# Kernel optimization log

Hardware: AMD Instinct MI355X
Metric: run time of the kernel (lower is better)

The kernel has to match this reference:

```python
import jax, jax.numpy as jnp
import numpy as np

D_MODEL = 512
N_HEADS = 8
D_K = D_MODEL // N_HEADS


def setup_inputs() -> dict:
    key = jax.random.key(0)
    ks = jax.random.split(key, 11)
    B, L, D = 2, 4096, D_MODEL
    s = 1.0 / np.sqrt(D)
    return {
        "q": jax.random.normal(ks[0], (B, L, D), jnp.float32),
        "k": jax.random.normal(ks[1], (B, L, D), jnp.float32),
        "v": jax.random.normal(ks[2], (B, L, D), jnp.float32),
        "Wq": jax.random.normal(ks[3], (D, D), jnp.float32) * s,
        "bq": jnp.zeros((D,), jnp.float32),
        "Wk": jax.random.normal(ks[4], (D, D), jnp.float32) * s,
        "bk": jnp.zeros((D,), jnp.float32),
        "Wv": jax.random.normal(ks[5], (D, D), jnp.float32) * s,
        "bv": jnp.zeros((D,), jnp.float32),
        "Wo": jax.random.normal(ks[6], (D, D), jnp.float32) * s,
        "bo": jnp.zeros((D,), jnp.float32),
    }


def reference(q, k, v, Wq, bq, Wk, bk, Wv, bv, Wo, bo):
    B, L, D = q.shape
    H, dk = N_HEADS, D_K
    # projections -> [B, H, L, dk]
    qh = (q @ Wq + bq).reshape(B, L, H, dk).transpose(0, 2, 1, 3)
    kh = (k @ Wk + bk).reshape(B, -1, H, dk).transpose(0, 2, 1, 3)
    vh = (v @ Wv + bv).reshape(B, -1, H, dk).transpose(0, 2, 1, 3)
    scores = jnp.einsum("bhqd,bhkd->bhqk", qh, kh) / jnp.sqrt(jnp.float32(dk))
    attn = jax.nn.softmax(scores, axis=-1)  # dropout: eval-mode identity
    ctx = jnp.einsum("bhqk,bhkd->bhqd", attn, vh)
    ctx = ctx.transpose(0, 2, 1, 3).reshape(B, L, D)
    return ctx @ Wo + bo
```

## Files before the change

kernel.cpp:

```cpp
#include <hip/hip_runtime.h>
#include <hip/hip_bf16.h>

#define NB 2
#define NL 4096
#define ND 512
#define NH 8
#define NDK 64
#define NM (NB * NL)
#define QSCALE 0.18033688011112042f

typedef short bf16x8_t __attribute__((ext_vector_type(8)));
typedef float f32x4_t __attribute__((ext_vector_type(4)));

static __device__ __forceinline__ unsigned short f2bs(float f) {
  union { float f; unsigned u; } c; c.f = f;
  unsigned r = c.u + 0x7fffu + ((c.u >> 16) & 1u);
  return (unsigned short)(r >> 16);
}
static __device__ __forceinline__ float bs2f(unsigned short s) {
  union { unsigned u; float f; } c; c.u = ((unsigned)s) << 16; return c.f;
}
static __device__ __forceinline__ unsigned pk_bf16(float a, float b) {
  union { __hip_bfloat162 h; unsigned u; } c;
  c.h = __float22bfloat162_rn(make_float2(a, b));
  return c.u;
}
static __device__ __forceinline__ unsigned cvt_pk_hw(float a, float b) {
  unsigned r;
  asm("v_cvt_pk_bf16_f32 %0, %1, %2" : "=v"(r) : "v"(a), "v"(b));
  return r;
}
static __device__ __forceinline__ void split_pk(float a, float b,
                                                unsigned& hw, unsigned& lw) {
  const unsigned short ha = f2bs(a), hb = f2bs(b);
  hw = (unsigned)ha | ((unsigned)hb << 16);
  lw = (unsigned)f2bs(a - bs2f(ha)) | ((unsigned)f2bs(b - bs2f(hb)) << 16);
}

struct WArgs {
  const float* W[4];
  unsigned short* Th[4];
  unsigned short* Tl[4];
};
__global__ __launch_bounds__(256)
void wsplit_kernel(WArgs a)
{
  const int z = blockIdx.z;
  const float* __restrict__ W = a.W[z];
  const int tid = threadIdx.x;
  const int n = blockIdx.x * 64 + (tid & 63);
  const int kb = blockIdx.y * 64 + (tid >> 6) * 16;
  unsigned short h[16], l[16];
#pragma unroll
  for (int u = 0; u < 16; ++u) {
    const float x = W[(size_t)(kb + u) * ND + n];
    h[u] = f2bs(x);
    l[u] = f2bs(x - bs2f(h[u]));
  }
  unsigned wh[8], wl[8];
#pragma unroll
  for (int p = 0; p < 8; ++p) {
    wh[p] = (unsigned)h[2 * p] | ((unsigned)h[2 * p + 1] << 16);
    wl[p] = (unsigned)l[2 * p] | ((unsigned)l[2 * p + 1] << 16);
  }
  unsigned short* th = a.Th[z] + (size_t)n * ND + kb;
  unsigned short* tl = a.Tl[z] + (size_t)n * ND + kb;
  *(uint4*)th = make_uint4(wh[0], wh[1], wh[2], wh[3]);
  *(uint4*)(th + 8) = make_uint4(wh[4], wh[5], wh[6], wh[7]);
  *(uint4*)tl = make_uint4(wl[0], wl[1], wl[2], wl[3]);
  *(uint4*)(tl + 8) = make_uint4(wl[4], wl[5], wl[6], wl[7]);
}

template <bool ASPLIT, int NJ, int OUTMODE, int WI, int WJ, bool AFP32, bool AMERGE>
__device__ __forceinline__ void gemm_core(
    const void* __restrict__ Ahi_, const unsigned short* __restrict__ Alo,
    const unsigned short* __restrict__ Bh, const unsigned short* __restrict__ Bl,
    const float* __restrict__ bias, unsigned short* __restrict__ outH,
    float* __restrict__ outF, int m0, int n0, float scale,
    const float* __restrict__ opA, const float* __restrict__ lpA)
{
  static_assert(!(ASPLIT && AFP32), "unsupported combo");
  static_assert(!(AFP32 && AMERGE), "unsupported combo");
  constexpr int WGC = NJ / WJ;
  static_assert((4 / WGC) * WI * 16 == 128, "wave grid must tile 128 rows");
  static_assert(OUTMODE == 1 || (WI == 4 && WJ == 4 && WGC == 2),
                "epilogues 0/2 assume 2x2 wave grid");

  __shared__ unsigned short AH[128][36];
  __shared__ unsigned short AL[ASPLIT ? 128 : 1][36];
  __shared__ unsigned short BHs[NJ * 16][36];
  __shared__ unsigned short BLs[NJ * 16][36];

  const int tid = threadIdx.x;
  const int lane = tid & 63, w = tid >> 6;
  const int m = lane & 15, quad = lane >> 4;
  const int wr = w / WGC, wc = w % WGC;
  const int r = tid >> 1, hf = (tid & 1) * 16;
  const int rb = (NJ == 8) ? (tid >> 1) : (tid >> 2);
  const int cb = (NJ == 8) ? ((tid & 1) * 16) : ((tid & 3) * 8);

  const unsigned short* aRow = nullptr;
  const float* aRowF = nullptr;
  if constexpr (AFP32)
    aRowF = (const float*)Ahi_ + (size_t)(m0 + r) * ND + hf;
  else if constexpr (!AMERGE)
    aRow = (const unsigned short*)Ahi_ + (size_t)(m0 + r) * ND + hf;
  const unsigned short* alRow =
      (ASPLIT && !AMERGE) ? (Alo + (size_t)(m0 + r) * ND + hf) : nullptr;
  const unsigned short* bhRow = Bh + (size_t)(n0 + rb) * ND + cb;
  const unsigned short* blRow = Bl + (size_t)(n0 + rb) * ND + cb;

  int abb = 0, all = 0;
  if constexpr (AMERGE) {
    abb = (m0 + r) >> 12;
    all = (m0 + r) & (NL - 1);
  }

  uint4 ra0, ra1;
  float4 fa0, fa1, fa2, fa3;
  if constexpr (AFP32) {
    fa0 = *(const float4*)(aRowF);
    fa1 = *(const float4*)(aRowF + 4);
    fa2 = *(const float4*)(aRowF + 8);
    fa3 = *(const float4*)(aRowF + 12);
  } else if constexpr (!AMERGE) {
    ra0 = *(const uint4*)(aRow);
    ra1 = *(const uint4*)(aRow + 8);
  }
  uint4 rl0, rl1;
  if constexpr (ASPLIT && !AMERGE) {
    rl0 = *(const uint4*)(alRow);
    rl1 = *(const uint4*)(alRow + 8);
  }
  uint4 rbh0 = *(const uint4*)(bhRow);
  uint4 rbl0 = *(const uint4*)(blRow);
  uint4 rbh1, rbl1;
  if constexpr (NJ == 8) {
    rbh1 = *(const uint4*)(bhRow + 8);
    rbl1 = *(const uint4*)(blRow + 8);
  }

  f32x4_t acc[WI][WJ];
#pragma unroll
  for (int i = 0; i < WI; ++i)
#pragma unroll
    for (int j = 0; j < WJ; ++j) acc[i][j] = (f32x4_t){0.f, 0.f, 0.f, 0.f};

  for (int k0 = 0; k0 < ND; k0 += 32) {
    float4 a00, a01, a02, a03, a10, a11, a12, a13;
    float li0, li1;
    if constexpr (AMERGE) {
      const int kk = k0 + hf;
      const int head = kk >> 6;
      const int d0 = kk & (NDK - 1);
      const size_t prow = (size_t)(abb * 8 + head) * NL + all;
      const float* p0 = opA + prow * NDK + d0;
      const float* p1 = p0 + (size_t)16 * NL * NDK;
      a00 = *(const float4*)p0;
      a01 = *(const float4*)(p0 + 4);
      a02 = *(const float4*)(p0 + 8);
      a03 = *(const float4*)(p0 + 12);
      a10 = *(const float4*)p1;
      a11 = *(const float4*)(p1 + 4);
      a12 = *(const float4*)(p1 + 8);
      a13 = *(const float4*)(p1 + 12);
      li0 = lpA[prow];
      li1 = lpA[prow + (size_t)16 * NL];
    }
    __syncthreads();
    if constexpr (AMERGE) {
      const float inv = 1.0f / (li0 + li1);
      uint4 uh0, ul0, uh1, ul1;
      split_pk((a00.x + a10.x) * inv, (a00.y + a10.y) * inv, uh0.x, ul0.x);
      split_pk((a00.z + a10.z) * inv, (a00.w + a10.w) * inv, uh0.y, ul0.y);
      split_pk((a01.x + a11.x) * inv, (a01.y + a11.y) * inv, uh0.z, ul0.z);
      split_pk((a01.z + a11.z) * inv, (a01.w + a11.w) * inv, uh0.w, ul0.w);
      split_pk((a02.x + a12.x) * inv, (a02.y + a12.y) * inv, uh1.x, ul1.x);
      split_pk((a02.z + a12.z) * inv, (a02.w + a12.w) * inv, uh1.y, ul1.y);
      split_pk((a03.x + a13.x) * inv, (a03.y + a13.y) * inv, uh1.z, ul1.z);
      split_pk((a03.z + a13.z) * inv, (a03.w + a13.w) * inv, uh1.w, ul1.w);
      *(uint4*)&AH[r][hf] = uh0;
      *(uint4*)&AH[r][hf + 8] = uh1;
      *(uint4*)&AL[r][hf] = ul0;
      *(uint4*)&AL[r][hf + 8] = ul1;
    } else if constexpr (AFP32) {
      uint4 ua0, ua1;
      ua0.x = pk_bf16(fa0.x, fa0.y);
      ua0.y = pk_bf16(fa0.z, fa0.w);
      ua0.z = pk_bf16(fa1.x, fa1.y);
      ua0.w = pk_bf16(fa1.z, fa1.w);
      ua1.x = pk_bf16(fa2.x, fa2.y);
      ua1.y = pk_bf16(fa2.z, fa2.w);
      ua1.z = pk_bf16(fa3.x, fa3.y);
      ua1.w = pk_bf16(fa3.z, fa3.w);
      *(uint4*)&AH[r][hf] = ua0;
      *(uint4*)&AH[r][hf + 8] = ua1;
    } else {
      *(uint4*)&AH[r][hf] = ra0;
      *(uint4*)&AH[r][hf + 8] = ra1;
    }
    if constexpr (ASPLIT && !AMERGE) {
      *(uint4*)&AL[r][hf] = rl0;
      *(uint4*)&AL[r][hf + 8] = rl1;
    }
    *(uint4*)&BHs[rb][cb] = rbh0;
    *(uint4*)&BLs[rb][cb] = rbl0;
    if constexpr (NJ == 8) {
      *(uint4*)&BHs[rb][cb + 8] = rbh1;
      *(uint4*)&BLs[rb][cb + 8] = rbl1;
    }
    if (k0 + 32 < ND) {
      const int kn = k0 + 32;
      if constexpr (AFP32) {
        fa0 = *(const float4*)(aRowF + kn);
        fa1 = *(const float4*)(aRowF + kn + 4);
        fa2 = *(const float4*)(aRowF + kn + 8);
        fa3 = *(const float4*)(aRowF + kn + 12);
      } else if constexpr (!AMERGE) {
        ra0 = *(const uint4*)(aRow + kn);
        ra1 = *(const uint4*)(aRow + kn + 8);
      }
      if constexpr (ASPLIT && !AMERGE) {
        rl0 = *(const uint4*)(alRow + kn);
        rl1 = *(const uint4*)(alRow + kn + 8);
      }
      rbh0 = *(const uint4*)(bhRow + kn);
      rbl0 = *(const uint4*)(blRow + kn);
      if constexpr (NJ == 8) {
        rbh1 = *(const uint4*)(bhRow + kn + 8);
        rbl1 = *(const uint4*)(blRow + kn + 8);
      }
    }
    __syncthreads();

    bf16x8_t ah[WI], al[ASPLIT ? WI : 1];
#pragma unroll
    for (int i = 0; i < WI; ++i) {
      ah[i] = *(const bf16x8_t*)&AH[wr * (WI * 16) + 16 * i + m][quad * 8];
      if constexpr (ASPLIT)
        al[i] = *(const bf16x8_t*)&AL[wr * (WI * 16) + 16 * i + m][quad * 8];
    }
#pragma unroll
    for (int j = 0; j < WJ; ++j) {
      const bf16x8_t bhj = *(const bf16x8_t*)&BHs[16 * (wc * WJ + j) + m][quad * 8];
      const bf16x8_t blj = *(const bf16x8_t*)&BLs[16 * (wc * WJ + j) + m][quad * 8];
#pragma unroll
      for (int i = 0; i < WI; ++i) {
        acc[i][j] = __builtin_amdgcn_mfma_f32_16x16x32_bf16(ah[i], bhj, acc[i][j], 0, 0, 0);
        acc[i][j] = __builtin_amdgcn_mfma_f32_16x16x32_bf16(ah[i], blj, acc[i][j], 0, 0, 0);
        if constexpr (ASPLIT)
          acc[i][j] = __builtin_amdgcn_mfma_f32_16x16x32_bf16(al[i], bhj, acc[i][j], 0, 0, 0);
      }
    }
  }

  if constexpr (OUTMODE == 1) {
#pragma unroll
    for (int i = 0; i < WI; ++i)
#pragma unroll
      for (int rr = 0; rr < 4; ++rr) {
        const int mg = m0 + wr * (WI * 16) + 16 * i + quad * 4 + rr;
#pragma unroll
        for (int j = 0; j < WJ; ++j) {
          const int n = n0 + 16 * (wc * WJ + j) + m;
          outF[(size_t)mg * ND + n] = (acc[i][j][rr] + bias[n]) * scale;
        }
      }
  } else if constexpr (OUTMODE == 0) {
    unsigned short* T = &BHs[0][0];
    const int bb = m0 >> 12;
#pragma unroll
    for (int p = 0; p < 4; ++p) {
      __syncthreads();
      if (wr == (p >> 1)) {
#pragma unroll
        for (int i2 = 0; i2 < 2; ++i2) {
          const int i = (p & 1) * 2 + i2;
#pragma unroll
          for (int j = 0; j < WJ; ++j) {
            const int n = wc * 64 + 16 * j + m;
            const float bv = bias[n0 + n];
#pragma unroll
            for (int rr = 0; rr < 4; ++rr)
              T[(16 * i2 + quad * 4 + rr) * 136 + n] =
                  f2bs((acc[i][j][rr] + bv) * scale);
          }
        }
      }
      __syncthreads();
      const int lr = tid >> 3;
      const int seg = tid & 7;
      const uint4 t0 = *(const uint4*)&T[lr * 136 + seg * 16];
      const uint4 t1 = *(const uint4*)&T[lr * 136 + seg * 16 + 8];
      const int ng = n0 + seg * 16;
      const int h = ng >> 6, d = ng & (NDK - 1);
      const int l = (m0 + p * 32 + lr) & (NL - 1);
      unsigned short* dp = outH + (((size_t)(bb * NH + h)) * NL + l) * NDK + d;
      *(uint4*)dp = t0;
      *(uint4*)(dp + 8) = t1;
    }
  } else {
    unsigned short* T = &BHs[0][0];
    const int bb = m0 >> 12;
    const int lbase = m0 & (NL - 1);
#pragma unroll
    for (int p = 0; p < 4; ++p) {
      __syncthreads();
      if (wr == (p >> 1)) {
#pragma unroll
        for (int i2 = 0; i2 < 2; ++i2) {
          const int i = (p & 1) * 2 + i2;
#pragma unroll
          for (int j = 0; j < WJ; ++j) {
            const int n = wc * 64 + 16 * j + m;
            const float bv = bias[n0 + n];
            const unsigned w0 = pk_bf16((acc[i][j][0] + bv) * scale,
                                        (acc[i][j][1] + bv) * scale);
            const unsigned w1 = pk_bf16((acc[i][j][2] + bv) * scale,
                                        (acc[i][j][3] + bv) * scale);
            *(uint2*)&T[n * 34 + 16 * i2 + quad * 4] = make_uint2(w0, w1);
          }
        }
      }
      __syncthreads();
      const int n = tid >> 1;
      const int l0 = (tid & 1) * 16;
      const uint4 t0 = *(const uint4*)&T[n * 34 + l0];
      const uint4 t1 = *(const uint4*)&T[n * 34 + l0 + 8];
      const int ng = n0 + n;
      const int h = ng >> 6, d = ng & (NDK - 1);
      unsigned short* dp =
          outH + (((size_t)(bb * NH + h)) * NDK + d) * NL + lbase + 32 * p + l0;
      *(uint4*)dp = t0;
      *(uint4*)(dp + 8) = t1;
    }
  }
}

struct ProjArgs {
  const float* A[3];
  const unsigned short* Bh[3];
  const unsigned short* Bl[3];
  const float* bias[3];
  unsigned short* out[3];
  float scale[3];
};
__global__ __launch_bounds__(256, 3)
void gemm_proj_kernel(ProjArgs a)
{
  const int z = blockIdx.z;
  if (z < 2)
    gemm_core<false, 8, 0, 4, 4, true, false>(
        a.A[z], nullptr, a.Bh[z], a.Bl[z], a.bias[z], a.out[z], nullptr,
        blockIdx.x * 128, blockIdx.y * 128, a.scale[z], nullptr, nullptr);
  else
    gemm_core<false, 8, 2, 4, 4, true, false>(
        a.A[2], nullptr, a.Bh[2], a.Bl[2], a.bias[2], a.out[2], nullptr,
        blockIdx.x * 128, blockIdx.y * 128, a.scale[2], nullptr, nullptr);
}
__global__ __launch_bounds__(256, 3)
void gemm_out_kernel(const float* __restrict__ opA, const float* __restrict__ lpA,
                     const unsigned short* __restrict__ Bh,
                     const unsigned short* __restrict__ Bl,
                     const float* __restrict__ bias, float* __restrict__ out)
{
  gemm_core<true, 4, 1, 2, 4, false, true>(
      nullptr, nullptr, Bh, Bl, bias, nullptr, out,
      blockIdx.x * 128, blockIdx.y * 64, 1.0f, opA, lpA);
}

__global__ __launch_bounds__(256, 2)
void attn_kernel(const unsigned short* __restrict__ qh, const unsigned short* __restrict__ kh,
                 const unsigned short* __restrict__ vt_g, float* __restrict__ op,
                 float* __restrict__ lp)
{
  __shared__ unsigned short Ks[2][64 * 64];
  __shared__ unsigned short Vt[2][64 * 64];

  const int tid = threadIdx.x;
  const int w = tid >> 6;
  const int lane = tid & 63;
  const int m = lane & 15;
  const int quad = lane >> 4;
  const int sw = m & 7;

  const int bid = blockIdx.x;
  const int half = bid & 1;
  const int qt = (bid >> 1) & 15;
  const int bh = bid >> 5;
  const int kt0 = half * 32, kt1 = kt0 + 32;
  const unsigned short* qb = qh + (size_t)bh * NL * NDK;
  const unsigned short* kb = kh + (size_t)bh * NL * NDK;
  const unsigned short* vb = vt_g + (size_t)bh * NDK * NL;

  bf16x8_t aq[4][2];
#pragma unroll
  for (int mt = 0; mt < 4; ++mt) {
    const unsigned short* qsrc =
        qb + (size_t)(qt * 256 + w * 64 + mt * 16 + m) * NDK + quad * 8;
    aq[mt][0] = *(const bf16x8_t*)(qsrc);
    aq[mt][1] = *(const bf16x8_t*)(qsrc + 32);
  }

  const short ob = (short)0x3F80;
  const bf16x8_t ones = {ob, ob, ob, ob, ob, ob, ob, ob};

  f32x4_t o[4][4];
#pragma unroll
  for (int mt = 0; mt < 4; ++mt)
#pragma unroll
    for (int nt = 0; nt < 4; ++nt) o[mt][nt] = (f32x4_t){0.f, 0.f, 0.f, 0.f};
  f32x4_t ol[4];
#pragma unroll
  for (int mt = 0; mt < 4; ++mt) ol[mt] = (f32x4_t){0.f, 0.f, 0.f, 0.f};

  const int kr = tid >> 2;
  const int kcb = tid & 3;
  const int kc = kcb * 16;
  const int r7 = kr & 7;
  const int st0 = kr * 64 + ((2 * kcb) ^ r7) * 8;
  const int st1 = kr * 64 + ((2 * kcb + 1) ^ r7) * 8;

  const int rowb = m * 64;
  const int ck0 = rowb + ((quad ^ sw) * 8);
  const int ck1 = rowb + (((quad + 4) ^ sw) * 8);
  const int vq = quad >> 1, vo = (quad & 1) * 4;
  const int va0[2] = { rowb + vo + (((0 + vq) ^ sw) * 8),
                       rowb + vo + (((4 + vq) ^ sw) * 8) };
  const int va1[2] = { rowb + vo + (((2 + vq) ^ sw) * 8),
                       rowb + vo + (((6 + vq) ^ sw) * 8) };

  const unsigned short* kptr = kb + (size_t)(kt0 * 64 + kr) * NDK + kc;
  const unsigned short* vptr = vb + (size_t)kr * NL + kt0 * 64 + kc;
  uint4 pk0 = *(const uint4*)kptr;
  uint4 pk1 = *(const uint4*)(kptr + 8);
  uint4 pv0 = *(const uint4*)vptr;
  uint4 pv1 = *(const uint4*)(vptr + 8);
  *(uint4*)&Ks[0][st0] = pk0;
  *(uint4*)&Ks[0][st1] = pk1;
  *(uint4*)&Vt[0][st0] = pv0;
  *(uint4*)&Vt[0][st1] = pv1;
  kptr += 64 * NDK;
  vptr += 64;
  pk0 = *(const uint4*)kptr;
  pk1 = *(const uint4*)(kptr + 8);
  pv0 = *(const uint4*)vptr;
  pv1 = *(const uint4*)(vptr + 8);
  __syncthreads();

#define ATTN_STEP(B, W, KT)                                                   \
  {                                                                           \
            \
    f32x4_t s[4][4];                                            \
    _Pragma("unroll")                                                         \
    for (int nt = 0; nt < 4; ++nt) {                                          \
      const bf16x8_t kf0 = *(const bf16x8_t*)&Ks[B][nt * 1024 + ck0];         \
      const bf16x8_t kf1 = *(const bf16x8_t*)&Ks[B][nt * 1024 + ck1];         \
      _Pragma("unroll")                                                       \
      for (int mt = 0; mt < 4; ++mt) {                                        \
        f32x4_t s_ = (f32x4_t){0.f, 0.f, 0.f, 0.f};                           \
        s_ = __builtin_amdgcn_mfma_f32_16x16x32_bf16(kf0, aq[mt][0], s_, 0, 0, 0); \
        s_ = __builtin_amdgcn_mfma_f32_16x16x32_bf16(kf1, aq[mt][1], s_, 0, 0, 0); \
        s[nt][mt] = s_;                                                       \
      }                                                                       \
    }                                                                         \
    __builtin_amdgcn_sched_barrier(0);   \
    _Pragma("unroll")                                                         \
    for (int c = 0; c < 2; ++c) {                                             \
      union U { bf16x8_t v; unsigned d[4]; };                                 \
      U pa[4];                                                                \
      _Pragma("unroll")                                                       \
      for (int mt = 0; mt < 4; ++mt) {                                        \
        pa[mt].d[0] = cvt_pk_hw(__builtin_amdgcn_exp2f(s[2 * c][mt][0]),      \
                                __builtin_amdgcn_exp2f(s[2 * c][mt][1]));     \
        pa[mt].d[1] = cvt_pk_hw(__builtin_amdgcn_exp2f(s[2 * c][mt][2]),      \
                                __builtin_amdgcn_exp2f(s[2 * c][mt][3]));     \
        pa[mt].d[2] = cvt_pk_hw(__builtin_amdgcn_exp2f(s[2 * c + 1][mt][0]),  \
                                __builtin_amdgcn_exp2f(s[2 * c + 1][mt][1])); \
        pa[mt].d[3] = cvt_pk_hw(__builtin_amdgcn_exp2f(s[2 * c + 1][mt][2]),  \
                                __builtin_amdgcn_exp2f(s[2 * c + 1][mt][3])); \
      }                                                                       \
      __builtin_amdgcn_s_setprio(1);                                          \
      _Pragma("unroll")                                                       \
      for (int nt = 0; nt < 4; ++nt) {                                        \
        union { bf16x8_t v; uint2 h[2]; } vf;                                 \
        vf.h[0] = *(const uint2*)&Vt[B][nt * 1024 + va0[c]];                  \
        vf.h[1] = *(const uint2*)&Vt[B][nt * 1024 + va1[c]];                  \
        _Pragma("unroll")                                                     \
        for (int mt = 0; mt < 4; ++mt)                                        \
          o[mt][nt] = __builtin_amdgcn_mfma_f32_16x16x32_bf16(pa[mt].v, vf.v, \
                                                              o[mt][nt], 0, 0, 0); \
      }                                                                       \
      _Pragma("unroll")                                                       \
      for (int mt = 0; mt < 4; ++mt)                                          \
        ol[mt] = __builtin_amdgcn_mfma_f32_16x16x32_bf16(pa[mt].v, ones,      \
                                                         ol[mt], 0, 0, 0);    \
      __builtin_amdgcn_s_setprio(0);                                          \
    }                                                                         \
    if ((KT) + 1 < kt1) {                                                     \
      *(uint4*)&Ks[W][st0] = pk0;                                             \
      *(uint4*)&Ks[W][st1] = pk1;                                             \
      *(uint4*)&Vt[W][st0] = pv0;                                             \
      *(uint4*)&Vt[W][st1] = pv1;                                             \
      if ((KT) + 2 < kt1) {                                                   \
        kptr += 64 * NDK;                                                     \
        vptr += 64;                                                           \
        pk0 = *(const uint4*)kptr;                                            \
        pk1 = *(const uint4*)(kptr + 8);                                      \
        pv0 = *(const uint4*)vptr;                                            \
        pv1 = *(const uint4*)(vptr + 8);                                      \
      }                                                                       \
      __syncthreads();                                                        \
    }                                                                         \
  }

  for (int kt = kt0; kt < kt1; kt += 2) {
    ATTN_STEP(0, 1, kt);
    ATTN_STEP(1, 0, kt + 1);
  }
#undef ATTN_STEP

  const size_t pbase = (size_t)(half * 16 + bh) * NL;
#pragma unroll
  for (int mt = 0; mt < 4; ++mt) {
    const int q0 = qt * 256 + w * 64 + mt * 16 + quad * 4;
    if (m == 0)
      *(float4*)&lp[pbase + q0] =
          make_float4(ol[mt][0], ol[mt][1], ol[mt][2], ol[mt][3]);
#pragma unroll
    for (int r = 0; r < 4; ++r) {
      float* dst = op + (pbase + q0 + r) * NDK;
#pragma unroll
      for (int nt = 0; nt < 4; ++nt) dst[16 * nt + m] = o[mt][nt][r];
    }
  }
}

extern "C" void kernel_launch(void* const* d_in, const int* in_sizes, int n_in,
                              void* d_out, int out_size, void* d_ws, size_t ws_size,
                              hipStream_t stream)
{
  const float* q  = (const float*)d_in[0];
  const float* k  = (const float*)d_in[1];
  const float* v  = (const float*)d_in[2];
  const float* Wq = (const float*)d_in[3];
  const float* bq = (const float*)d_in[4];
  const float* Wk = (const float*)d_in[5];
  const float* bk = (const float*)d_in[6];
  const float* Wv = (const float*)d_in[7];
  const float* bv = (const float*)d_in[8];
  const float* Wo = (const float*)d_in[9];
  const float* bo = (const float*)d_in[10];

  const size_t PLANE = (size_t)NM * ND;
  unsigned short* wt = (unsigned short*)d_ws;
  unsigned short* qhp = wt + 8 * (size_t)ND * ND;
  unsigned short* khp = qhp + PLANE;
  unsigned short* vtp = khp + PLANE;
  float* op = (float*)(vtp + PLANE);
  float* lp = op + 2 * (size_t)16 * NL * NDK;

  unsigned short* wth[4], *wtl[4];
  for (int i = 0; i < 4; ++i) {
    wth[i] = wt + (size_t)(2 * i) * ND * ND;
    wtl[i] = wt + (size_t)(2 * i + 1) * ND * ND;
  }

  WArgs wa;
  wa.W[0] = Wq; wa.W[1] = Wk; wa.W[2] = Wv; wa.W[3] = Wo;
  for (int i = 0; i < 4; ++i) { wa.Th[i] = wth[i]; wa.Tl[i] = wtl[i]; }
  wsplit_kernel<<<dim3(8, 8, 4), 256, 0, stream>>>(wa);

  ProjArgs pa;
  pa.A[0] = q; pa.A[1] = k; pa.A[2] = v;
  pa.Bh[0] = wth[0]; pa.Bl[0] = wtl[0];
  pa.Bh[1] = wth[1]; pa.Bl[1] = wtl[1];
  pa.Bh[2] = wth[2]; pa.Bl[2] = wtl[2];
  pa.bias[0] = bq; pa.bias[1] = bk; pa.bias[2] = bv;
  pa.out[0] = qhp; pa.out[1] = khp; pa.out[2] = vtp;
  pa.scale[0] = QSCALE; pa.scale[1] = 1.0f; pa.scale[2] = 1.0f;
  gemm_proj_kernel<<<dim3(NM / 128, ND / 128, 3), 256, 0, stream>>>(pa);

  attn_kernel<<<dim3(NB * NH * (NL / 256) * 2), 256, 0, stream>>>(qhp, khp, vtp, op, lp);

  gemm_out_kernel<<<dim3(NM / 128, ND / 64), 256, 0, stream>>>(
      op, lp, wth[3], wtl[3], bo, (float*)d_out);
}
```

Before: 243.5 us.

## Stream B tiles directly into double-buffered LDS via global_load_lds

```diff
diff --git a/kernel.cpp b/kernel.cpp
--- a/kernel.cpp
+++ b/kernel.cpp
@@ -35,6 +35,11 @@
   const unsigned short ha = f2bs(a), hb = f2bs(b);
   hw = (unsigned)ha | ((unsigned)hb << 16);
   lw = (unsigned)f2bs(a - bs2f(ha)) | ((unsigned)f2bs(b - bs2f(hb)) << 16);
+}
+static __device__ __forceinline__ void gload_lds16(const void* g, void* l) {
+  __builtin_amdgcn_global_load_lds(
+      (const __attribute__((address_space(1))) unsigned*)g,
+      (__attribute__((address_space(3))) unsigned*)l, 16, 0, 0);
 }
 
 struct WArgs {
@@ -85,19 +90,21 @@
   static_assert((4 / WGC) * WI * 16 == 128, "wave grid must tile 128 rows");
   static_assert(OUTMODE == 1 || (WI == 4 && WJ == 4 && WGC == 2),
                 "epilogues 0/2 assume 2x2 wave grid");
+  static_assert((NJ * 16) % 64 == 0, "B tile must split into 16-row groups x 4 waves");
 
   __shared__ unsigned short AH[128][36];
   __shared__ unsigned short AL[ASPLIT ? 128 : 1][36];
-  __shared__ unsigned short BHs[NJ * 16][36];
-  __shared__ unsigned short BLs[NJ * 16][36];
+  __shared__ unsigned short BS[2][2][NJ * 16][32];
 
   const int tid = threadIdx.x;
   const int lane = tid & 63, w = tid >> 6;
   const int m = lane & 15, quad = lane >> 4;
   const int wr = w / WGC, wc = w % WGC;
   const int r = tid >> 1, hf = (tid & 1) * 16;
-  const int rb = (NJ == 8) ? (tid >> 1) : (tid >> 2);
-  const int cb = (NJ == 8) ? ((tid & 1) * 16) : ((tid & 3) * 8);
+
+  constexpr int GPW = (NJ * 16) / 64;
+  const int bln = lane >> 2;
+  const int blc = (lane & 3) * 8;
 
   const unsigned short* aRow = nullptr;
   const float* aRowF = nullptr;
@@ -107,14 +114,25 @@
     aRow = (const unsigned short*)Ahi_ + (size_t)(m0 + r) * ND + hf;
   const unsigned short* alRow =
       (ASPLIT && !AMERGE) ? (Alo + (size_t)(m0 + r) * ND + hf) : nullptr;
-  const unsigned short* bhRow = Bh + (size_t)(n0 + rb) * ND + cb;
-  const unsigned short* blRow = Bl + (size_t)(n0 + rb) * ND + cb;
 
   int abb = 0, all = 0;
   if constexpr (AMERGE) {
     abb = (m0 + r) >> 12;
     all = (m0 + r) & (NL - 1);
   }
+
+  auto issueB = [&](int k0s, int buf) {
+#pragma unroll
+    for (int t = 0; t < GPW; ++t) {
+      const int g = w * GPW + t;
+      const unsigned short* gh = Bh + (size_t)(n0 + g * 16 + bln) * ND + k0s + blc;
+      const unsigned short* gl = Bl + (size_t)(n0 + g * 16 + bln) * ND + k0s + blc;
+      gload_lds16(gh, &BS[buf][0][g * 16][0]);
+      gload_lds16(gl, &BS[buf][1][g * 16][0]);
+    }
+  };
+
+  issueB(0, 0);
 
   uint4 ra0, ra1;
   float4 fa0, fa1, fa2, fa3;
@@ -132,13 +150,6 @@
     rl0 = *(const uint4*)(alRow);
     rl1 = *(const uint4*)(alRow + 8);
   }
-  uint4 rbh0 = *(const uint4*)(bhRow);
-  uint4 rbl0 = *(const uint4*)(blRow);
-  uint4 rbh1, rbl1;
-  if constexpr (NJ == 8) {
-    rbh1 = *(const uint4*)(bhRow + 8);
-    rbl1 = *(const uint4*)(blRow + 8);
-  }
 
   f32x4_t acc[WI][WJ];
 #pragma unroll
@@ -147,6 +158,7 @@
     for (int j = 0; j < WJ; ++j) acc[i][j] = (f32x4_t){0.f, 0.f, 0.f, 0.f};
 
   for (int k0 = 0; k0 < ND; k0 += 32) {
+    const int cur = (k0 >> 5) & 1;
     float4 a00, a01, a02, a03, a10, a11, a12, a13;
     float li0, li1;
     if constexpr (AMERGE) {
@@ -203,12 +215,6 @@
       *(uint4*)&AL[r][hf] = rl0;
       *(uint4*)&AL[r][hf + 8] = rl1;
     }
-    *(uint4*)&BHs[rb][cb] = rbh0;
-    *(uint4*)&BLs[rb][cb] = rbl0;
-    if constexpr (NJ == 8) {
-      *(uint4*)&BHs[rb][cb + 8] = rbh1;
-      *(uint4*)&BLs[rb][cb + 8] = rbl1;
-    }
     if (k0 + 32 < ND) {
       const int kn = k0 + 32;
       if constexpr (AFP32) {
@@ -224,14 +230,9 @@
         rl0 = *(const uint4*)(alRow + kn);
         rl1 = *(const uint4*)(alRow + kn + 8);
       }
-      rbh0 = *(const uint4*)(bhRow + kn);
-      rbl0 = *(const uint4*)(blRow + kn);
-      if constexpr (NJ == 8) {
-        rbh1 = *(const uint4*)(bhRow + kn + 8);
-        rbl1 = *(const uint4*)(blRow + kn + 8);
-      }
     }
     __syncthreads();
+    if (k0 + 32 < ND) issueB(k0 + 32, cur ^ 1);
 
     bf16x8_t ah[WI], al[ASPLIT ? WI : 1];
 #pragma unroll
@@ -242,8 +243,9 @@
     }
 #pragma unroll
     for (int j = 0; j < WJ; ++j) {
-      const bf16x8_t bhj = *(const bf16x8_t*)&BHs[16 * (wc * WJ + j) + m][quad * 8];
-      const bf16x8_t blj = *(const bf16x8_t*)&BLs[16 * (wc * WJ + j) + m][quad * 8];
+      const int bR = 16 * (wc * WJ + j) + m;
+      const bf16x8_t bhj = *(const bf16x8_t*)&BS[cur][0][bR][quad * 8];
+      const bf16x8_t blj = *(const bf16x8_t*)&BS[cur][1][bR][quad * 8];
 #pragma unroll
       for (int i = 0; i < WI; ++i) {
         acc[i][j] = __builtin_amdgcn_mfma_f32_16x16x32_bf16(ah[i], bhj, acc[i][j], 0, 0, 0);
@@ -267,7 +269,7 @@
         }
       }
   } else if constexpr (OUTMODE == 0) {
-    unsigned short* T = &BHs[0][0];
+    unsigned short* T = &BS[0][0][0][0];
     const int bb = m0 >> 12;
 #pragma unroll
     for (int p = 0; p < 4; ++p) {
@@ -300,7 +302,7 @@
       *(uint4*)(dp + 8) = t1;
     }
   } else {
-    unsigned short* T = &BHs[0][0];
+    unsigned short* T = &BS[0][0][0][0];
     const int bb = m0 >> 12;
     const int lbase = m0 & (NL - 1);
 #pragma unroll
```

New measurement: 278.6 us. +14.4%, slower.
